# Optimization experiments

Measured on AMD Instinct MI355X. Metric: run time of the kernel, lower is better.

## Reference

```python
import jax, jax.numpy as jnp
import numpy as np

DIM = 256
HEADS = 8
WSZ = (2, 7, 7)
SSZ = (1, 3, 3)
EPS = 1e-5


def _rel_index(wsz):
    wt, wh, ww = wsz
    coords = np.stack(np.meshgrid(np.arange(wt), np.arange(wh), np.arange(ww), indexing='ij'))
    coords = coords.reshape(3, -1)  # (3, N)
    rel = coords[:, :, None] - coords[:, None, :]  # (3, N, N)
    rel = rel.transpose(1, 2, 0).copy()  # (N, N, 3)
    rel[:, :, 0] += wt - 1
    rel[:, :, 1] += wh - 1
    rel[:, :, 2] += ww - 1
    rel[:, :, 0] *= (2 * wh - 1) * (2 * ww - 1)
    rel[:, :, 1] *= (2 * ww - 1)
    return rel.sum(-1)  # (N, N) int


def _attn_mask_np(T, H, W, wsz, ssz):
    wt, wh, ww = wsz
    st, sh, sw = ssz
    img = np.zeros((T, H, W), np.int32)
    cnt = 0
    for t in (slice(0, -wt), slice(-wt, -st), slice(-st, None)):
        for h in (slice(0, -wh), slice(-wh, -sh), slice(-sh, None)):
            for w in (slice(0, -ww), slice(-ww, -sw), slice(-sw, None)):
                img[t, h, w] = cnt
                cnt += 1
    m = img.reshape(T // wt, wt, H // wh, wh, W // ww, ww)
    m = m.transpose(0, 2, 4, 1, 3, 5).reshape(-1, wt * wh * ww)  # (nW, N)
    diff = m[:, :, None] - m[:, None, :]
    return np.where(diff != 0, -100.0, 0.0).astype(np.float32)  # (nW, N, N)


def _ln(x, w, b):
    mu = x.mean(-1, keepdims=True)
    var = jnp.mean((x - mu) ** 2, -1, keepdims=True)
    return (x - mu) * jax.lax.rsqrt(var + EPS) * w + b


def _window_partition(x, wsz):
    B, T, H, W, C = x.shape
    wt, wh, ww = wsz
    x = x.reshape(B, T // wt, wt, H // wh, wh, W // ww, ww, C)
    x = x.transpose(0, 1, 3, 5, 2, 4, 6, 7)
    return x.reshape(-1, wt * wh * ww, C)


def _window_reverse(xw, wsz, B, T, H, W):
    wt, wh, ww = wsz
    C = xw.shape[-1]
    x = xw.reshape(B, T // wt, H // wh, W // ww, wt, wh, ww, C)
    x = x.transpose(0, 1, 4, 2, 5, 3, 6, 7)
    return x.reshape(B, T, H, W, C)


def setup_inputs() -> dict:
    key = jax.random.key(0)
    ks = jax.random.split(key, 8)
    B, T, H, W = 2, 8, 56, 56
    d = DIM
    hid = 4 * d
    rpe_rows = (2 * WSZ[0] - 1) * (2 * WSZ[1] - 1) * (2 * WSZ[2] - 1)
    s = 0.02
    return {
        'x': jax.random.normal(ks[0], (B, T, H, W, d), jnp.float32),
        'norm1_w': jnp.ones((d,), jnp.float32),
        'norm1_b': jnp.zeros((d,), jnp.float32),
        'qkv_w': jax.random.normal(ks[1], (3 * d, d), jnp.float32) * s,
        'qkv_b': jnp.zeros((3 * d,), jnp.float32),
        'proj_w': jax.random.normal(ks[2], (d, d), jnp.float32) * s,
        'proj_b': jnp.zeros((d,), jnp.float32),
        'rpe_table': jax.random.normal(ks[3], (rpe_rows, HEADS), jnp.float32) * s,
        'norm2_w': jnp.ones((d,), jnp.float32),
        'norm2_b': jnp.zeros((d,), jnp.float32),
        'fc1_w': jax.random.normal(ks[4], (hid, d), jnp.float32) * s,
        'fc1_b': jnp.zeros((hid,), jnp.float32),
        'fc2_w': jax.random.normal(ks[5], (d, hid), jnp.float32) * s,
        'fc2_b': jnp.zeros((d,), jnp.float32),
    }


def reference(x, norm1_w, norm1_b, qkv_w, qkv_b, proj_w, proj_b, rpe_table,
              norm2_w, norm2_b, fc1_w, fc1_b, fc2_w, fc2_b):
    B, T, H, W, C = x.shape
    wt, wh, ww = WSZ
    N = wt * wh * ww
    hd = C // HEADS
    scale = hd ** -0.5

    shortcut = x
    h = _ln(x, norm1_w, norm1_b)
    # shifted branch: cyclic roll + mask
    h = jnp.roll(h, (-SSZ[0], -SSZ[1], -SSZ[2]), axis=(1, 2, 3))
    mask = jnp.asarray(_attn_mask_np(T, H, W, WSZ, SSZ))  # (nW, N, N)
    nW = mask.shape[0]

    xw = _window_partition(h, WSZ)  # (B*nW, N, C)
    Bw = xw.shape[0]

    qkv = xw @ qkv_w.T + qkv_b  # (Bw, N, 3C)
    qkv = qkv.reshape(Bw, N, 3, HEADS, hd).transpose(2, 0, 3, 1, 4)
    q, k, v = qkv[0], qkv[1], qkv[2]  # (Bw, H, N, hd)

    idx = _rel_index(WSZ)  # (N, N)
    bias = rpe_table[idx].transpose(2, 0, 1)  # (heads, N, N)

    attn = jnp.einsum('bhnd,bhmd->bhnm', q * scale, k) + bias[None]
    attn = attn.reshape(B, nW, HEADS, N, N) + mask[None, :, None]
    attn = jax.nn.softmax(attn, axis=-1).reshape(Bw, HEADS, N, N)

    out = jnp.einsum('bhnm,bhmd->bhnd', attn, v)
    out = out.transpose(0, 2, 1, 3).reshape(Bw, N, C)
    out = out @ proj_w.T + proj_b

    out = _window_reverse(out, WSZ, B, T, H, W)
    out = jnp.roll(out, (SSZ[0], SSZ[1], SSZ[2]), axis=(1, 2, 3))

    x = shortcut + out
    h2 = _ln(x, norm2_w, norm2_b)
    h2 = jax.nn.gelu(h2 @ fc1_w.T + fc1_b, approximate=False)
    h2 = h2 @ fc2_w.T + fc2_b
    return x + h2
```

## Files before the change

### kernel.cpp

```cpp
#include <hip/hip_runtime.h>
#include <math.h>

#define TOKENS 50176
#define NWIN   512
#define MR     392

typedef __attribute__((ext_vector_type(8))) short short8;
typedef __attribute__((ext_vector_type(4))) float f32x4;
typedef __attribute__((ext_vector_type(4))) unsigned short us4;

__device__ __forceinline__ unsigned short f2bf(float f) {
    unsigned int u = __builtin_bit_cast(unsigned int, f);
    u += 0x7fffu + ((u >> 16) & 1);
    return (unsigned short)(u >> 16);
}

__device__ __forceinline__ void gll16(const void* g, void* l) {
    __builtin_amdgcn_global_load_lds(
        (const __attribute__((address_space(1))) unsigned int*)g,
        (__attribute__((address_space(3))) unsigned int*)l, 16, 0, 0);
}

__device__ __forceinline__ int win_token_to_flat(int u) {
    int g = u / 98;
    int n = u - g * 98;
    int bb  = g >> 8;
    int rem = g & 255;
    int tb = rem >> 6, hb = (rem >> 3) & 7, wb = rem & 7;
    int dt = n / 49;
    int r2 = n - dt * 49;
    int dh = r2 / 7, dw = r2 - dh * 7;
    int t = tb * 2 + dt, h = hb * 7 + dh, w = wb * 7 + dw;
    int ts = (t + 1) & 7;
    int hs = h + 3; if (hs >= 56) hs -= 56;
    int wsx = w + 3; if (wsx >= 56) wsx -= 56;
    return ((bb * 8 + ts) * 56 + hs) * 56 + wsx;
}

__global__ __launch_bounds__(256) void cvt_kernel(
        const float* __restrict__ src, unsigned short* __restrict__ dst, int n) {
    int i = blockIdx.x * 256 + threadIdx.x;
    if (i < n) dst[i] = f2bf(src[i]);
}

__global__ __launch_bounds__(256) void bm_kernel(
        const float* __restrict__ rpe, float* __restrict__ bm) {
    int i = blockIdx.x * 256 + threadIdx.x;
    int c  = i % 112;
    int t1 = i / 112;
    int r  = t1 % 112;
    int t2 = t1 / 112;
    int head = t2 & 7;
    int cls  = t2 >> 3;
    float val;
    if (c >= 98) {
        val = -1e30f;
    } else if (r >= 98) {
        val = 0.f;
    } else {
        int dt = r / 49, rr = r - dt * 49, dh = rr / 7, dw = rr - dh * 7;
        int dt2 = c / 49, cc = c - dt2 * 49, dh2 = cc / 7, dw2 = cc - dh2 * 7;
        int rt  = (cls & 4) ? (dt  == 0 ? 1 : 2) : 0;
        int rh  = (cls & 2) ? (dh  <  4 ? 1 : 2) : 0;
        int rw  = (cls & 1) ? (dw  <  4 ? 1 : 2) : 0;
        int rt2 = (cls & 4) ? (dt2 == 0 ? 1 : 2) : 0;
        int rh2 = (cls & 2) ? (dh2 <  4 ? 1 : 2) : 0;
        int rw2 = (cls & 1) ? (dw2 <  4 ? 1 : 2) : 0;
        int reg1 = rt * 9 + rh * 3 + rw, reg2 = rt2 * 9 + rh2 * 3 + rw2;
        int idx = (dt - dt2 + 1) * 169 + (dh - dh2 + 6) * 13 + (dw - dw2 + 6);
        val = rpe[idx * 8 + head] + ((reg1 == reg2) ? 0.f : -100.f);
    }
    bm[i] = val;
}

template<bool GATHER>
__global__ __launch_bounds__(256) void ln_kernel(
        const float* __restrict__ x, const float* __restrict__ w,
        const float* __restrict__ b, unsigned short* __restrict__ out) {
    int token = blockIdx.x * 4 + (threadIdx.x >> 6);
    int lane  = threadIdx.x & 63;
    size_t so = GATHER ? (size_t)win_token_to_flat(token) * 256
                       : (size_t)token * 256;
    float4 v = *(const float4*)(x + so + lane * 4);
    float sum = v.x + v.y + v.z + v.w;
#pragma unroll
    for (int o = 32; o > 0; o >>= 1) sum += __shfl_xor(sum, o, 64);
    float mu = sum * (1.f / 256.f);
    float d0 = v.x - mu, d1 = v.y - mu, d2 = v.z - mu, d3 = v.w - mu;
    float var = d0 * d0 + d1 * d1 + d2 * d2 + d3 * d3;
#pragma unroll
    for (int o = 32; o > 0; o >>= 1) var += __shfl_xor(var, o, 64);
    float rstd = rsqrtf(var * (1.f / 256.f) + 1e-5f);
    float4 gw = *(const float4*)(w + lane * 4);
    float4 gb = *(const float4*)(b + lane * 4);
    us4 pk = { f2bf(d0 * rstd * gw.x + gb.x), f2bf(d1 * rstd * gw.y + gb.y),
               f2bf(d2 * rstd * gw.z + gb.z), f2bf(d3 * rstd * gw.w + gb.w) };
    *(us4*)(out + (size_t)token * 256 + lane * 4) = pk;
}

template<int EPI>
__global__ __launch_bounds__(256) void gemm_v2(
        const unsigned short* __restrict__ A, const unsigned short* __restrict__ B,
        const float* __restrict__ bias, const float* __restrict__ res,
        void* __restrict__ Cout, int N, int K) {
    __shared__ __attribute__((aligned(16))) unsigned short Asm[128 * 32];
    __shared__ __attribute__((aligned(16))) unsigned short Bsm[128 * 32];
    int tid = threadIdx.x;
    int wave = tid >> 6, lane = tid & 63;
    int bid = blockIdx.x;
    int row0 = (bid % MR) * 128;
    int col0 = (bid / MR) * 128;
    int wr = (wave >> 1) * 64;
    int wc = (wave & 1) * 64;

    f32x4 acc[4][4] = {};

    int srow = tid >> 2;
    int sc = (tid & 3) ^ ((srow >> 1) & 3);
    const unsigned short* Ag0 = A + (size_t)(row0 + srow) * K + sc * 8;
    const unsigned short* Ag1 = A + (size_t)(row0 + 64 + srow) * K + sc * 8;
    const unsigned short* Bg0 = B + (size_t)(col0 + srow) * K + sc * 8;
    const unsigned short* Bg1 = B + (size_t)(col0 + 64 + srow) * K + sc * 8;
    unsigned short* Al0 = Asm + tid * 8;
    unsigned short* Al1 = Asm + (256 + tid) * 8;
    unsigned short* Bl0 = Bsm + tid * 8;
    unsigned short* Bl1 = Bsm + (256 + tid) * 8;

    int fm = lane & 15, fq = lane >> 4;

    for (int k0 = 0; k0 < K; k0 += 32) {
        __syncthreads();
        gll16(Ag0 + k0, Al0);
        gll16(Ag1 + k0, Al1);
        gll16(Bg0 + k0, Bl0);
        gll16(Bg1 + k0, Bl1);
        __syncthreads();
        short8 tf[4], wf[4];
#pragma unroll
        for (int mt = 0; mt < 4; ++mt) {
            int r = wr + mt * 16 + fm;
            tf[mt] = *(const short8*)&Asm[(r * 4 + (fq ^ ((r >> 1) & 3))) * 8];
        }
#pragma unroll
        for (int nt = 0; nt < 4; ++nt) {
            int r = wc + nt * 16 + fm;
            wf[nt] = *(const short8*)&Bsm[(r * 4 + (fq ^ ((r >> 1) & 3))) * 8];
        }
#pragma unroll
        for (int mt = 0; mt < 4; ++mt)
#pragma unroll
            for (int nt = 0; nt < 4; ++nt)
                acc[mt][nt] = __builtin_amdgcn_mfma_f32_16x16x32_bf16(
                    wf[nt], tf[mt], acc[mt][nt], 0, 0, 0);
    }

    int token0 = row0 + wr + fm;
    int wcol0  = col0 + wc + fq * 4;
    float4 bs[4];
#pragma unroll
    for (int nt = 0; nt < 4; ++nt)
        bs[nt] = *(const float4*)&bias[wcol0 + nt * 16];

#pragma unroll
    for (int mt = 0; mt < 4; ++mt) {
        int token = token0 + mt * 16;
        if (EPI == 1) {
            float* C = (float*)Cout;
            size_t tbase = (size_t)win_token_to_flat(token) * 256;
#pragma unroll
            for (int nt = 0; nt < 4; ++nt) {
                size_t off = tbase + wcol0 + nt * 16;
                float4 r4 = *(const float4*)&res[off];
                float4 o4 = { r4.x + acc[mt][nt][0] + bs[nt].x,
                              r4.y + acc[mt][nt][1] + bs[nt].y,
                              r4.z + acc[mt][nt][2] + bs[nt].z,
                              r4.w + acc[mt][nt][3] + bs[nt].w };
                *(float4*)&C[off] = o4;
            }
        } else {
            unsigned short* C = (unsigned short*)Cout;
            size_t tbase = (size_t)token * N;
#pragma unroll
            for (int nt = 0; nt < 4; ++nt) {
                float v0 = acc[mt][nt][0] + bs[nt].x;
                float v1 = acc[mt][nt][1] + bs[nt].y;
                float v2 = acc[mt][nt][2] + bs[nt].z;
                float v3 = acc[mt][nt][3] + bs[nt].w;
                if (EPI == 0) {
                    float mul = (wcol0 + nt * 16 < 256) ? 0.17677669529663687f : 1.f;
                    v0 *= mul; v1 *= mul; v2 *= mul; v3 *= mul;
                } else {
                    v0 = 0.5f * v0 * (1.f + erff(v0 * 0.70710678118654752f));
                    v1 = 0.5f * v1 * (1.f + erff(v1 * 0.70710678118654752f));
                    v2 = 0.5f * v2 * (1.f + erff(v2 * 0.70710678118654752f));
                    v3 = 0.5f * v3 * (1.f + erff(v3 * 0.70710678118654752f));
                }
                us4 pk = { f2bf(v0), f2bf(v1), f2bf(v2), f2bf(v3) };
                *(us4*)&C[tbase + wcol0 + nt * 16] = pk;
            }
        }
    }
}

__global__ __launch_bounds__(256) void fc2_kernel(
        const unsigned short* __restrict__ A, const unsigned short* __restrict__ W,
        const float* __restrict__ bias, const float* __restrict__ res,
        float* __restrict__ out) {
    __shared__ __attribute__((aligned(16))) unsigned short As[64 * 32];
    __shared__ __attribute__((aligned(16))) unsigned short Bs[256 * 32];
    int tid = threadIdx.x, wave = tid >> 6, lane = tid & 63;
    int fm = lane & 15, fq = lane >> 4;
    int row0 = blockIdx.x * 64;

    f32x4 acc[4][4] = {};

    int srow = tid >> 2;
    int sca = (tid & 3) ^ ((srow >> 1) & 3);
    const unsigned short* Asrc = A + (size_t)(row0 + srow) * 1024 + sca * 8;
    const unsigned short* Bsrc[4];
#pragma unroll
    for (int i = 0; i < 4; ++i) {
        int s = i * 256 + tid;
        int br = s >> 2;
        int c = (s & 3) ^ ((br >> 1) & 3);
        Bsrc[i] = W + (size_t)br * 1024 + c * 8;
    }

    for (int k0 = 0; k0 < 1024; k0 += 32) {
        __syncthreads();
        gll16(Asrc + k0, As + tid * 8);
#pragma unroll
        for (int i = 0; i < 4; ++i)
            gll16(Bsrc[i] + k0, Bs + (i * 256 + tid) * 8);
        __syncthreads();
        short8 tf[4], wf[4];
#pragma unroll
        for (int mt = 0; mt < 4; ++mt) {
            int r = mt * 16 + fm;
            tf[mt] = *(const short8*)&As[(r * 4 + (fq ^ ((r >> 1) & 3))) * 8];
        }
#pragma unroll
        for (int nt = 0; nt < 4; ++nt) {
            int r = wave * 64 + nt * 16 + fm;
            wf[nt] = *(const short8*)&Bs[(r * 4 + (fq ^ ((r >> 1) & 3))) * 8];
        }
#pragma unroll
        for (int mt = 0; mt < 4; ++mt)
#pragma unroll
            for (int nt = 0; nt < 4; ++nt)
                acc[mt][nt] = __builtin_amdgcn_mfma_f32_16x16x32_bf16(
                    wf[nt], tf[mt], acc[mt][nt], 0, 0, 0);
    }

    int wcol0 = wave * 64 + fq * 4;
    float4 bs[4];
#pragma unroll
    for (int nt = 0; nt < 4; ++nt)
        bs[nt] = *(const float4*)&bias[wcol0 + nt * 16];
#pragma unroll
    for (int mt = 0; mt < 4; ++mt) {
        size_t tbase = (size_t)(row0 + mt * 16 + fm) * 256;
#pragma unroll
        for (int nt = 0; nt < 4; ++nt) {
            size_t off = tbase + wcol0 + nt * 16;
            float4 r4 = *(const float4*)&res[off];
            float4 o4 = { r4.x + acc[mt][nt][0] + bs[nt].x,
                          r4.y + acc[mt][nt][1] + bs[nt].y,
                          r4.z + acc[mt][nt][2] + bs[nt].z,
                          r4.w + acc[mt][nt][3] + bs[nt].w };
            *(float4*)&out[off] = o4;
        }
    }
}

__global__ __launch_bounds__(256) void attn_mfma_kernel(
        const unsigned short* __restrict__ qkv, const float* __restrict__ bm,
        unsigned short* __restrict__ out) {
    __shared__ __attribute__((aligned(16))) unsigned short Vt[32][136];
    __shared__ __attribute__((aligned(16))) unsigned short Pw[4][16][136];
    int blk = blockIdx.x;
    int g = blk >> 3, head = blk & 7;
    int tid = threadIdx.x, wave = tid >> 6, lane = tid & 63;

    for (int i = tid; i < 32 * 30; i += 256) {
        int d = i / 30, c = 98 + (i - d * 30);
        Vt[d][c] = 0;
    }
    const unsigned short* vbase = qkv + (size_t)g * 98 * 768 + 512 + head * 32;
    for (int i = tid; i < 98 * 16; i += 256) {
        int n = i >> 4, dp = i & 15;
        unsigned int val = *(const unsigned int*)(vbase + (size_t)n * 768 + dp * 2);
        Vt[dp * 2][n]     = (unsigned short)val;
        Vt[dp * 2 + 1][n] = (unsigned short)(val >> 16);
    }
    {
        int m = lane >> 2, c = 112 + (lane & 3) * 4;
        *(unsigned long long*)&Pw[wave][m][c] = 0ULL;
    }
    __syncthreads();

    const unsigned short* qbase = qkv + (size_t)g * 98 * 768 + head * 32;
    const unsigned short* kbase = qbase + 256;
    int rem = g & 255;
    int cls = (((rem >> 6) == 3) << 2) | (((((rem >> 3) & 7)) == 7) << 1) | ((rem & 7) == 7);
    const float* bmh = bm + (size_t)(cls * 8 + head) * 112 * 112;

    int fm = lane & 15, fq = lane >> 4;
    int fk = fq * 8;
    unsigned short* obase = out + (size_t)g * 98 * 256 + head * 32;

    for (int s = wave; s < 7; s += 4) {
        int m0 = s * 16;
        int arow = m0 + fm; if (arow > 97) arow = 97;
        short8 af = *(const short8*)(qbase + (size_t)arow * 768 + fk);
        f32x4 S[7];
        f32x4 z = {0.f, 0.f, 0.f, 0.f};
#pragma unroll
        for (int j = 0; j < 7; ++j) {
            int krow = j * 16 + fm; if (krow > 97) krow = 97;
            short8 kf = *(const short8*)(kbase + (size_t)krow * 768 + fk);
            S[j] = __builtin_amdgcn_mfma_f32_16x16x32_bf16(af, kf, z, 0, 0, 0);
        }
        const float* bmrow = bmh + (m0 + fq * 4) * 112 + fm;
#pragma unroll
        for (int j = 0; j < 7; ++j)
#pragma unroll
            for (int v = 0; v < 4; ++v)
                S[j][v] += bmrow[v * 112 + j * 16];
        float inv[4];
#pragma unroll
        for (int v = 0; v < 4; ++v) {
            float m_ = S[0][v];
#pragma unroll
            for (int j = 1; j < 7; ++j) m_ = fmaxf(m_, S[j][v]);
#pragma unroll
            for (int o = 1; o < 16; o <<= 1) m_ = fmaxf(m_, __shfl_xor(m_, o, 64));
            float t = 0.f;
#pragma unroll
            for (int j = 0; j < 7; ++j) { S[j][v] = __expf(S[j][v] - m_); t += S[j][v]; }
#pragma unroll
            for (int o = 1; o < 16; o <<= 1) t += __shfl_xor(t, o, 64);
            inv[v] = 1.f / t;
        }
#pragma unroll
        for (int j = 0; j < 7; ++j)
#pragma unroll
            for (int v = 0; v < 4; ++v)
                Pw[wave][fq * 4 + v][j * 16 + fm] = f2bf(S[j][v]);
        f32x4 O0 = {0.f, 0.f, 0.f, 0.f}, O1 = {0.f, 0.f, 0.f, 0.f};
#pragma unroll
        for (int ks = 0; ks < 4; ++ks) {
            short8 pf = *(const short8*)&Pw[wave][fm][ks * 32 + fk];
            short8 v0 = *(const short8*)&Vt[fm][ks * 32 + fk];
            short8 v1 = *(const short8*)&Vt[16 + fm][ks * 32 + fk];
            O0 = __builtin_amdgcn_mfma_f32_16x16x32_bf16(pf, v0, O0, 0, 0, 0);
            O1 = __builtin_amdgcn_mfma_f32_16x16x32_bf16(pf, v1, O1, 0, 0, 0);
        }
#pragma unroll
        for (int v = 0; v < 4; ++v) {
            int row = m0 + fq * 4 + v;
            if (row < 98) {
                obase[(size_t)row * 256 + fm]      = f2bf(O0[v] * inv[v]);
                obase[(size_t)row * 256 + 16 + fm] = f2bf(O1[v] * inv[v]);
            }
        }
    }
}

extern "C" void kernel_launch(void* const* d_in, const int* in_sizes, int n_in,
                              void* d_out, int out_size, void* d_ws, size_t ws_size,
                              hipStream_t stream) {
    const float* x     = (const float*)d_in[0];
    const float* n1w   = (const float*)d_in[1];
    const float* n1b   = (const float*)d_in[2];
    const float* qkvw  = (const float*)d_in[3];
    const float* qkvb  = (const float*)d_in[4];
    const float* projw = (const float*)d_in[5];
    const float* projb = (const float*)d_in[6];
    const float* rpe   = (const float*)d_in[7];
    const float* n2w   = (const float*)d_in[8];
    const float* n2b   = (const float*)d_in[9];
    const float* fc1w  = (const float*)d_in[10];
    const float* fc1b  = (const float*)d_in[11];
    const float* fc2w  = (const float*)d_in[12];
    const float* fc2b  = (const float*)d_in[13];
    float* out = (float*)d_out;

    unsigned short* wqkv  = (unsigned short*)d_ws;
    unsigned short* wproj = wqkv + 768 * 256;
    unsigned short* wfc1  = wproj + 256 * 256;
    unsigned short* wfc2  = wfc1 + 1024 * 256;
    float* bm = (float*)(wfc2 + 256 * 1024);
    unsigned short* actA  = (unsigned short*)(bm + 8 * 8 * 112 * 112);
    unsigned short* attnO = actA + (size_t)TOKENS * 256;
    unsigned short* qkv_bf = attnO + (size_t)TOKENS * 256;
    unsigned short* fc1o = qkv_bf;

    bm_kernel<<<8 * 8 * 112 * 112 / 256, 256, 0, stream>>>(rpe, bm);
    cvt_kernel<<<(768 * 256 + 255) / 256, 256, 0, stream>>>(qkvw, wqkv, 768 * 256);
    cvt_kernel<<<(256 * 256 + 255) / 256, 256, 0, stream>>>(projw, wproj, 256 * 256);
    cvt_kernel<<<(1024 * 256 + 255) / 256, 256, 0, stream>>>(fc1w, wfc1, 1024 * 256);
    cvt_kernel<<<(256 * 1024 + 255) / 256, 256, 0, stream>>>(fc2w, wfc2, 256 * 1024);

    ln_kernel<true><<<TOKENS / 4, 256, 0, stream>>>(x, n1w, n1b, actA);
    gemm_v2<0><<<MR * 6, 256, 0, stream>>>(actA, wqkv, qkvb, nullptr, qkv_bf, 768, 256);
    attn_mfma_kernel<<<NWIN * 8, 256, 0, stream>>>(qkv_bf, bm, attnO);
    gemm_v2<1><<<MR * 2, 256, 0, stream>>>(attnO, wproj, projb, x, out, 256, 256);
    ln_kernel<false><<<TOKENS / 4, 256, 0, stream>>>(out, n2w, n2b, actA);
    gemm_v2<2><<<MR * 8, 256, 0, stream>>>(actA, wfc1, fc1b, nullptr, fc1o, 1024, 256);
    fc2_kernel<<<TOKENS / 64, 256, 0, stream>>>(fc1o, wfc2, fc2b, out, out);
}
```

Before: 433.0 us.

## Merge weight conversions, use tanh-form GELU, route fc2 through gemm_v2

Folds the four weight-conversion launches into one kernel and replaces the erf-based GELU with a sigmoid (tanh-equivalent) approximation using fast exp and reciprocal. It also hoists the q-scale multiplier out of the inner loop and drops the dedicated fc2 kernel in favour of a new gemm_v2<3> epilogue with a plain row-major residual add. The approximate GELU differs from the exact erf form the reference uses and may loosen accuracy. The fc2 GEMM now uses gemm_v2's tiling (128-row tiles, MR*2 blocks) instead of 64-row full-width tiles.

```diff
diff --git a/kernel.cpp b/kernel.cpp
--- a/kernel.cpp
+++ b/kernel.cpp
@@ -13,6 +13,13 @@
     unsigned int u = __builtin_bit_cast(unsigned int, f);
     u += 0x7fffu + ((u >> 16) & 1);
     return (unsigned short)(u >> 16);
+}
+
+__device__ __forceinline__ float fast_gelu(float x) {
+    float x2 = x * x;
+    float z = x * __builtin_fmaf(x2, 0.0713548162726f, 1.59576912161f);
+    float s = __builtin_amdgcn_rcpf(1.f + __expf(-z));
+    return x * s;
 }
 
 __device__ __forceinline__ void gll16(const void* g, void* l) {
@@ -37,10 +44,18 @@
     return ((bb * 8 + ts) * 56 + hs) * 56 + wsx;
 }
 
-__global__ __launch_bounds__(256) void cvt_kernel(
-        const float* __restrict__ src, unsigned short* __restrict__ dst, int n) {
+__global__ __launch_bounds__(256) void cvt_all_kernel(
+        const float* __restrict__ qkvw, const float* __restrict__ projw,
+        const float* __restrict__ fc1w, const float* __restrict__ fc2w,
+        unsigned short* __restrict__ dst) {
     int i = blockIdx.x * 256 + threadIdx.x;
-    if (i < n) dst[i] = f2bf(src[i]);
+    const float* src;
+    int off;
+    if (i < 196608)      { src = qkvw;  off = i; }
+    else if (i < 262144) { src = projw; off = i - 196608; }
+    else if (i < 524288) { src = fc1w;  off = i - 262144; }
+    else                 { src = fc2w;  off = i - 524288; }
+    dst[i] = f2bf(src[off]);
 }
 
 __global__ __launch_bounds__(256) void bm_kernel(
@@ -160,13 +175,16 @@
 #pragma unroll
     for (int nt = 0; nt < 4; ++nt)
         bs[nt] = *(const float4*)&bias[wcol0 + nt * 16];
+    float qmul = (EPI == 0 && col0 < 256) ? 0.17677669529663687f : 1.f;
 
 #pragma unroll
     for (int mt = 0; mt < 4; ++mt) {
         int token = token0 + mt * 16;
-        if (EPI == 1) {
+        if (EPI == 1 || EPI == 3) {
             float* C = (float*)Cout;
-            size_t tbase = (size_t)win_token_to_flat(token) * 256;
+            size_t tbase = (EPI == 1)
+                ? (size_t)win_token_to_flat(token) * 256
+                : (size_t)token * 256;
 #pragma unroll
             for (int nt = 0; nt < 4; ++nt) {
                 size_t off = tbase + wcol0 + nt * 16;
@@ -187,88 +205,14 @@
                 float v2 = acc[mt][nt][2] + bs[nt].z;
                 float v3 = acc[mt][nt][3] + bs[nt].w;
                 if (EPI == 0) {
-                    float mul = (wcol0 + nt * 16 < 256) ? 0.17677669529663687f : 1.f;
-                    v0 *= mul; v1 *= mul; v2 *= mul; v3 *= mul;
+                    v0 *= qmul; v1 *= qmul; v2 *= qmul; v3 *= qmul;
                 } else {
-                    v0 = 0.5f * v0 * (1.f + erff(v0 * 0.70710678118654752f));
-                    v1 = 0.5f * v1 * (1.f + erff(v1 * 0.70710678118654752f));
-                    v2 = 0.5f * v2 * (1.f + erff(v2 * 0.70710678118654752f));
-                    v3 = 0.5f * v3 * (1.f + erff(v3 * 0.70710678118654752f));
+                    v0 = fast_gelu(v0); v1 = fast_gelu(v1);
+                    v2 = fast_gelu(v2); v3 = fast_gelu(v3);
                 }
                 us4 pk = { f2bf(v0), f2bf(v1), f2bf(v2), f2bf(v3) };
                 *(us4*)&C[tbase + wcol0 + nt * 16] = pk;
             }
-        }
-    }
-}
-
-__global__ __launch_bounds__(256) void fc2_kernel(
-        const unsigned short* __restrict__ A, const unsigned short* __restrict__ W,
-        const float* __restrict__ bias, const float* __restrict__ res,
-        float* __restrict__ out) {
-    __shared__ __attribute__((aligned(16))) unsigned short As[64 * 32];
-    __shared__ __attribute__((aligned(16))) unsigned short Bs[256 * 32];
-    int tid = threadIdx.x, wave = tid >> 6, lane = tid & 63;
-    int fm = lane & 15, fq = lane >> 4;
-    int row0 = blockIdx.x * 64;
-
-    f32x4 acc[4][4] = {};
-
-    int srow = tid >> 2;
-    int sca = (tid & 3) ^ ((srow >> 1) & 3);
-    const unsigned short* Asrc = A + (size_t)(row0 + srow) * 1024 + sca * 8;
-    const unsigned short* Bsrc[4];
-#pragma unroll
-    for (int i = 0; i < 4; ++i) {
-        int s = i * 256 + tid;
-        int br = s >> 2;
-        int c = (s & 3) ^ ((br >> 1) & 3);
-        Bsrc[i] = W + (size_t)br * 1024 + c * 8;
-    }
-
-    for (int k0 = 0; k0 < 1024; k0 += 32) {
-        __syncthreads();
-        gll16(Asrc + k0, As + tid * 8);
-#pragma unroll
-        for (int i = 0; i < 4; ++i)
-            gll16(Bsrc[i] + k0, Bs + (i * 256 + tid) * 8);
-        __syncthreads();
-        short8 tf[4], wf[4];
-#pragma unroll
-        for (int mt = 0; mt < 4; ++mt) {
-            int r = mt * 16 + fm;
-            tf[mt] = *(const short8*)&As[(r * 4 + (fq ^ ((r >> 1) & 3))) * 8];
-        }
-#pragma unroll
-        for (int nt = 0; nt < 4; ++nt) {
-            int r = wave * 64 + nt * 16 + fm;
-            wf[nt] = *(const short8*)&Bs[(r * 4 + (fq ^ ((r >> 1) & 3))) * 8];
-        }
-#pragma unroll
-        for (int mt = 0; mt < 4; ++mt)
-#pragma unroll
-            for (int nt = 0; nt < 4; ++nt)
-                acc[mt][nt] = __builtin_amdgcn_mfma_f32_16x16x32_bf16(
-                    wf[nt], tf[mt], acc[mt][nt], 0, 0, 0);
-    }
-
-    int wcol0 = wave * 64 + fq * 4;
-    float4 bs[4];
-#pragma unroll
-    for (int nt = 0; nt < 4; ++nt)
-        bs[nt] = *(const float4*)&bias[wcol0 + nt * 16];
-#pragma unroll
-    for (int mt = 0; mt < 4; ++mt) {
-        size_t tbase = (size_t)(row0 + mt * 16 + fm) * 256;
-#pragma unroll
-        for (int nt = 0; nt < 4; ++nt) {
-            size_t off = tbase + wcol0 + nt * 16;
-            float4 r4 = *(const float4*)&res[off];
-            float4 o4 = { r4.x + acc[mt][nt][0] + bs[nt].x,
-                          r4.y + acc[mt][nt][1] + bs[nt].y,
-                          r4.z + acc[mt][nt][2] + bs[nt].z,
-                          r4.w + acc[mt][nt][3] + bs[nt].w };
-            *(float4*)&out[off] = o4;
         }
     }
 }
@@ -386,7 +330,8 @@
     const float* fc2b  = (const float*)d_in[13];
     float* out = (float*)d_out;
 
-    unsigned short* wqkv  = (unsigned short*)d_ws;
+    unsigned short* wbase = (unsigned short*)d_ws;
+    unsigned short* wqkv  = wbase;
     unsigned short* wproj = wqkv + 768 * 256;
     unsigned short* wfc1  = wproj + 256 * 256;
     unsigned short* wfc2  = wfc1 + 1024 * 256;
@@ -397,10 +342,7 @@
     unsigned short* fc1o = qkv_bf;
 
     bm_kernel<<<8 * 8 * 112 * 112 / 256, 256, 0, stream>>>(rpe, bm);
-    cvt_kernel<<<(768 * 256 + 255) / 256, 256, 0, stream>>>(qkvw, wqkv, 768 * 256);
-    cvt_kernel<<<(256 * 256 + 255) / 256, 256, 0, stream>>>(projw, wproj, 256 * 256);
-    cvt_kernel<<<(1024 * 256 + 255) / 256, 256, 0, stream>>>(fc1w, wfc1, 1024 * 256);
-    cvt_kernel<<<(256 * 1024 + 255) / 256, 256, 0, stream>>>(fc2w, wfc2, 256 * 1024);
+    cvt_all_kernel<<<786432 / 256, 256, 0, stream>>>(qkvw, projw, fc1w, fc2w, wbase);
 
     ln_kernel<true><<<TOKENS / 4, 256, 0, stream>>>(x, n1w, n1b, actA);
     gemm_v2<0><<<MR * 6, 256, 0, stream>>>(actA, wqkv, qkvb, nullptr, qkv_bf, 768, 256);
@@ -408,5 +350,5 @@
     gemm_v2<1><<<MR * 2, 256, 0, stream>>>(attnO, wproj, projb, x, out, 256, 256);
     ln_kernel<false><<<TOKENS / 4, 256, 0, stream>>>(out, n2w, n2b, actA);
     gemm_v2<2><<<MR * 8, 256, 0, stream>>>(actA, wfc1, fc1b, nullptr, fc1o, 1024, 256);
-    fc2_kernel<<<TOKENS / 64, 256, 0, stream>>>(fc1o, wfc2, fc2b, out, out);
-}
+    gemm_v2<3><<<MR * 2, 256, 0, stream>>>(fc1o, wfc2, fc2b, out, out, 256, 1024);
+}
```

Result: faster. 415.9 us (-3.9%).
